# Kernel tuning notes

Measured on AMD Instinct MI355X. Metric: run time of the kernel, lower is better.

The kernel has to match this reference:

```python
import jax, jax.numpy as jnp
import numpy as np

TOP_K = 2  # config.moe_config.top_k


def setup_inputs() -> dict:
    key = jax.random.key(0)
    k0, k1, k2, k3 = jax.random.split(key, 4)
    T, H, I, E = 8192, 2048, 1408, 8  # tokens, hidden, moe_intermediate, experts
    x = jax.random.normal(k0, (T, H), jnp.float32)
    router_weight = jax.random.normal(k1, (E, H), jnp.float32) * 0.02
    gate_up_proj = jax.random.normal(k2, (E, H, 2 * I), jnp.float32) * 0.02
    down_proj = jax.random.normal(k3, (E, I, H), jnp.float32) * 0.02
    return {"x": x, "router_weight": router_weight,
            "gate_up_proj": gate_up_proj, "down_proj": down_proj}


def _moe_forward(x, router_weight, gate_up_proj, down_proj):
    # Router: fp32 gating linear (no bias), softmax over experts, top-k,
    # then scatter the top-k softmax weights into a dense [T, E] gate tensor
    # (topk_version=False path of Router.top_k_softmax).
    T = x.shape[0]
    E = router_weight.shape[0]
    logits = x.astype(jnp.float32) @ router_weight.T            # [T, E]
    probs = jax.nn.softmax(logits, axis=-1)                      # [T, E]
    topk_w, topk_idx = jax.lax.top_k(probs, TOP_K)               # [T, k]
    gates = jnp.zeros_like(logits).at[
        jnp.arange(T)[:, None], topk_idx].set(topk_w)            # [T, E] sparse gates

    # Grouped expert MLP (GroupedMLP): merged gate/up GEMM, SwiGLU, down GEMM.
    # Dispatch/permute + grouped GEMM + weighted combine is mathematically
    # out[t] = sum_e gates[t, e] * MLP_e(x[t]); expressed here as a fixed loop
    # over the small expert set with masked accumulation (jit-friendly).
    out = jnp.zeros_like(x)
    for e in range(E):
        gu = x @ gate_up_proj[e]                                 # [T, 2I]
        g, u = jnp.split(gu, 2, axis=-1)
        h = (jax.nn.silu(g) * u) @ down_proj[e]                  # [T, H]
        out = out + gates[:, e:e + 1].astype(x.dtype) * h
    return out


def reference(x, router_weight, gate_up_proj, down_proj):
    return _moe_forward(x, router_weight, gate_up_proj, down_proj)
```

## Files before the change

kernel.cpp:

```cpp
#include <hip/hip_runtime.h>
#include <hip/hip_bf16.h>
#include <cstdint>
#include <cstddef>

#define T_TOK 8192
#define H_DIM 2048
#define I_DIM 1408
#define E_NUM 8
#define BM 128
#define BK 64
#define ROWS_CAP (2 * T_TOK + E_NUM * BM)
#define MAX_MT (ROWS_CAP / BM)
#define NT1 (I_DIM / 64)
#define NT2 (H_DIM / 128)

typedef __attribute__((ext_vector_type(8))) short short8;
typedef __attribute__((ext_vector_type(4))) float f32x4;
typedef __attribute__((ext_vector_type(8))) unsigned short bf16x8;
typedef __attribute__((ext_vector_type(4))) unsigned short bf16x4;
typedef __attribute__((ext_vector_type(8))) _Float16 h16x8;

static __device__ __forceinline__ unsigned short f2bf(float f) {
  unsigned u = __float_as_uint(f);
  u += 0x7FFFu + ((u >> 16) & 1u);
  return (unsigned short)(u >> 16);
}

static __device__ __forceinline__ void gld_lds16(const void* g, void* l) {
  __builtin_amdgcn_global_load_lds(
      (__attribute__((address_space(1))) unsigned int*)g,
      (__attribute__((address_space(3))) unsigned int*)l, 16, 0, 0);
}

template <int G>
static __device__ __forceinline__ void remap_tile(int bid, int nb, int nt_cols,
                                                  int& m_t, int& n_t) {
  int chunk = nb >> 3;
  int wg = (bid & 7) * chunk + (bid >> 3);
  int grp = wg / (nt_cols * G);
  int rem = wg % (nt_cols * G);
  n_t = rem / G;
  m_t = grp * G + rem % G;
}

__global__ __launch_bounds__(256) void router_kernel(
    const float* __restrict__ x, const float* __restrict__ rw,
    unsigned short* __restrict__ xb,
    int* __restrict__ topk_idx, float* __restrict__ topk_w, int* __restrict__ meta) {
  int t = blockIdx.x * 4 + (threadIdx.x >> 6);
  int lane = threadIdx.x & 63;
  const float* xr = x + (size_t)t * H_DIM;
  unsigned short* xbr = xb + (size_t)t * H_DIM;
  float acc[E_NUM];
#pragma unroll
  for (int e = 0; e < E_NUM; e++) acc[e] = 0.f;
  for (int j = lane * 4; j < H_DIM; j += 256) {
    f32x4 v = *(const f32x4*)(xr + j);
    bf16x4 b;
#pragma unroll
    for (int u = 0; u < 4; u++) b[u] = f2bf(v[u]);
    *(bf16x4*)(xbr + j) = b;
#pragma unroll
    for (int e = 0; e < E_NUM; e++) {
      f32x4 w = *(const f32x4*)(rw + e * H_DIM + j);
      acc[e] += v[0] * w[0] + v[1] * w[1] + v[2] * w[2] + v[3] * w[3];
    }
  }
#pragma unroll
  for (int e = 0; e < E_NUM; e++) {
    float v = acc[e];
#pragma unroll
    for (int s = 32; s > 0; s >>= 1) v += __shfl_xor(v, s);
    acc[e] = v;
  }
  if (lane == 0) {
    int i0 = 0;
#pragma unroll
    for (int e = 1; e < E_NUM; e++) if (acc[e] > acc[i0]) i0 = e;
    int i1 = (i0 == 0) ? 1 : 0;
#pragma unroll
    for (int e = 0; e < E_NUM; e++) if (e != i0 && acc[e] > acc[i1]) i1 = e;
    float mx = acc[0];
#pragma unroll
    for (int e = 1; e < E_NUM; e++) mx = fmaxf(mx, acc[e]);
    float sum = 0.f, p[E_NUM];
#pragma unroll
    for (int e = 0; e < E_NUM; e++) { p[e] = expf(acc[e] - mx); sum += p[e]; }
    float inv = 1.f / sum;
    topk_idx[t * 2] = i0;  topk_idx[t * 2 + 1] = i1;
    topk_w[t * 2] = p[i0] * inv;  topk_w[t * 2 + 1] = p[i1] * inv;
    atomicAdd(&meta[i0], 1);
    atomicAdd(&meta[i1], 1);
  }
}

__global__ void scan_kernel(int* __restrict__ meta, int* __restrict__ row_token) {
  __shared__ int s_off[E_NUM + 1];
  if (threadIdx.x == 0) {
    int o = 0, nt = 0;
    for (int e = 0; e < E_NUM; e++) {
      meta[16 + e] = o; s_off[e] = o;
      int c = meta[e];
      int mtc = (c + BM - 1) / BM;
      for (int m = 0; m < mtc; m++) { meta[64 + nt] = e; meta[256 + nt] = o + m * BM; nt++; }
      o += mtc * BM;
      meta[8 + e] = 0;
    }
    meta[16 + E_NUM] = o; s_off[E_NUM] = o;
    meta[32] = nt;
  }
  __syncthreads();
  for (int e = 0; e < E_NUM; e++) {
    int lo = s_off[e] + meta[e], hi = s_off[e + 1];
    for (int r = lo + (int)threadIdx.x; r < hi; r += 64) row_token[r] = -1;
  }
}

__global__ __launch_bounds__(256) void bucket_kernel(
    const int* __restrict__ topk_idx, int* __restrict__ meta,
    int* __restrict__ row_token, int* __restrict__ tok2row) {
  int i = blockIdx.x * 256 + threadIdx.x;
  if (i >= 2 * T_TOK) return;
  int e = topk_idx[i];
  int pos = atomicAdd(&meta[8 + e], 1);
  int r = meta[16 + e] + pos;
  row_token[r] = i >> 1;
  tok2row[i] = r;
}

__global__ __launch_bounds__(256) void tcvt2_kernel(
    const float* __restrict__ wgu, const float* __restrict__ wdn,
    unsigned short* __restrict__ wgu_t, unsigned short* __restrict__ wd_t) {
  __shared__ alignas(16) float st[128 * 128];
  int z = blockIdx.z;
  const float* src; unsigned short* dst; int R, C;
  if (z < E_NUM) {
    R = H_DIM; C = 2 * I_DIM;
    src = wgu + (size_t)z * R * C;  dst = wgu_t + (size_t)z * R * C;
  } else {
    R = I_DIM; C = H_DIM;
    src = wdn + (size_t)(z - E_NUM) * R * C;  dst = wd_t + (size_t)(z - E_NUM) * R * C;
  }
  int c0 = blockIdx.x * 128, r0 = blockIdx.y * 128;
  if (c0 >= C || r0 >= R) return;
  int tid = threadIdx.x, l = tid & 63, w = tid >> 6;
#pragma unroll
  for (int i = 0; i < 16; i++) {
    int r = i * 8 + w * 2 + (l >> 5);
    int key = (r & 7) ^ ((r >> 3) & 7);
    int c4 = (l & 31) ^ key;
    gld_lds16(src + (size_t)(r0 + r) * C + c0 + c4 * 4,
              (char*)st + (i * 8 + w * 2) * 512);
  }
  __syncthreads();
  int ca = tid & 15, cg = tid >> 4;
#pragma unroll
  for (int it = 0; it < 8; it++) {
    int c = it * 16 + cg;
    bf16x8 o;
#pragma unroll
    for (int j = 0; j < 8; j++) {
      int r = ca * 8 + j;
      int key = (r & 7) ^ ((r >> 3) & 7);
      o[j] = f2bf(st[r * 128 + (((c >> 2) ^ key) << 2) + (c & 3)]);
    }
    *(bf16x8*)(dst + (size_t)(c0 + c) * R + r0 + ca * 8) = o;
  }
}

__global__ __launch_bounds__(256) void gemm1_kernel(
    const unsigned short* __restrict__ xb,
    const unsigned short* __restrict__ wgu,
    unsigned short* __restrict__ hbuf,
    const int* __restrict__ row_token, const int* __restrict__ meta) {
  int m_t, n_t;
  remap_tile<4>(blockIdx.x, NT1 * MAX_MT, NT1, m_t, n_t);
  if (m_t >= meta[32]) return;
  int e = meta[64 + m_t];
  int row0 = meta[256 + m_t];
  int n0h = n_t * 64;

  __shared__ alignas(16) char smem[65536];

  int tid = threadIdx.x, lane = tid & 63, wid = tid >> 6;
  const unsigned short* asrc[4];
  const unsigned short* bsrc[4];
  {
    const unsigned short* wb = wgu + (size_t)e * (2 * (size_t)I_DIM) * H_DIM;
#pragma unroll
    for (int i = 0; i < 4; i++) {
      int r = i * 32 + (tid >> 3);
      int ch = ((tid & 7) ^ (r & 7)) * 8;
      int tok = row_token[row0 + r];
      if (tok < 0) tok = 0;
      asrc[i] = xb + (size_t)tok * H_DIM + ch;
      int wr = (r < 64) ? (n0h + r) : (I_DIM + n0h + (r - 64));
      bsrc[i] = wb + (size_t)wr * H_DIM + ch;
    }
  }
  f32x4 acc[4][4] = {};
  int mrow = (wid >> 1) * 64 + (lane & 15);
  int brow = (wid & 1) * 64 + (lane & 15);

#define STAGE1(buf, kof_)                                                     \
  {                                                                           \
    int kof = (kof_);                                                         \
    char* b = smem + (buf) * 32768;                                           \
    _Pragma("unroll") for (int i = 0; i < 4; i++) {                           \
      gld_lds16(asrc[i] + kof, b + i * 4096 + wid * 1024);                    \
      gld_lds16(bsrc[i] + kof, b + 16384 + i * 4096 + wid * 1024);            \
    }                                                                         \
  }

  constexpr int NK1 = H_DIM / BK;
  STAGE1(0, 0);
  STAGE1(1, BK);
  for (int kt = 0; kt < NK1; kt++) {
    int cur = kt & 1;
    if (kt + 1 < NK1) { asm volatile("s_waitcnt vmcnt(8)" ::: "memory"); }
    else              { asm volatile("s_waitcnt vmcnt(0)" ::: "memory"); }
    __builtin_amdgcn_s_barrier();
    const unsigned short* sA = (const unsigned short*)(smem + cur * 32768);
    const unsigned short* sB = sA + 8192;
#pragma unroll
    for (int kk = 0; kk < 2; kk++) {
      int krd = ((kk * 4 + (lane >> 4)) ^ (lane & 7)) * 8;
      short8 af[4], bf[4];
#pragma unroll
      for (int f = 0; f < 4; f++) {
        af[f] = *(const short8*)(sA + (mrow + f * 16) * BK + krd);
        bf[f] = *(const short8*)(sB + (brow + f * 16) * BK + krd);
      }
#pragma unroll
      for (int fm = 0; fm < 4; fm++)
#pragma unroll
        for (int fn = 0; fn < 4; fn++)
          acc[fm][fn] = __builtin_amdgcn_mfma_f32_16x16x32_bf16(af[fm], bf[fn], acc[fm][fn], 0, 0, 0);
    }
    asm volatile("" ::: "memory");
    __builtin_amdgcn_s_barrier();
    asm volatile("" ::: "memory");
    if (kt + 2 < NK1) STAGE1(cur, (kt + 2) * BK);
  }

  float* xw = (float*)smem + (wid >> 1) * 4096;
  if (wid & 1) {
#pragma unroll
    for (int fm = 0; fm < 4; fm++)
#pragma unroll
      for (int r = 0; r < 4; r++) {
        int mloc = fm * 16 + (lane >> 4) * 4 + r;
#pragma unroll
        for (int fn = 0; fn < 4; fn++)
          xw[mloc * 64 + fn * 16 + (lane & 15)] = acc[fm][fn][r];
      }
  }
  __syncthreads();
  if (!(wid & 1)) {
    int mbase = row0 + (wid >> 1) * 64;
#pragma unroll
    for (int fm = 0; fm < 4; fm++)
#pragma unroll
      for (int r = 0; r < 4; r++) {
        int mloc = fm * 16 + (lane >> 4) * 4 + r;
        size_t rbase = (size_t)(mbase + mloc) * I_DIM + n0h;
#pragma unroll
        for (int fn = 0; fn < 4; fn++) {
          float g = acc[fm][fn][r];
          float u = xw[mloc * 64 + fn * 16 + (lane & 15)];
          float hv = (g / (1.f + __expf(-g))) * u;
          hbuf[rbase + fn * 16 + (lane & 15)] = f2bf(hv);
        }
      }
  }
}

__global__ __launch_bounds__(256) void gemm2_kernel(
    const unsigned short* __restrict__ hbuf,
    const unsigned short* __restrict__ wd,
    _Float16* __restrict__ part,
    const int* __restrict__ meta) {
  int m_t, n_t;
  remap_tile<8>(blockIdx.x, NT2 * MAX_MT, NT2, m_t, n_t);
  if (m_t >= meta[32]) return;
  int e = meta[64 + m_t];
  int row0 = meta[256 + m_t];
  int n0 = n_t * 128;

  __shared__ alignas(16) char smem[65536];

  int tid = threadIdx.x, lane = tid & 63, wid = tid >> 6;
  const unsigned short* asrc[4];
  const unsigned short* bsrc[4];
  {
    const unsigned short* wb = wd + (size_t)e * (size_t)H_DIM * I_DIM;
#pragma unroll
    for (int i = 0; i < 4; i++) {
      int r = i * 32 + (tid >> 3);
      int ch = ((tid & 7) ^ (r & 7)) * 8;
      asrc[i] = hbuf + (size_t)(row0 + r) * I_DIM + ch;
      bsrc[i] = wb + (size_t)(n0 + r) * I_DIM + ch;
    }
  }
  f32x4 acc[4][4] = {};
  int mrow = (wid >> 1) * 64 + (lane & 15);
  int brow = (wid & 1) * 64 + (lane & 15);

  constexpr int NK2 = I_DIM / BK;
  STAGE1(0, 0);
  STAGE1(1, BK);
  for (int kt = 0; kt < NK2; kt++) {
    int cur = kt & 1;
    if (kt + 1 < NK2) { asm volatile("s_waitcnt vmcnt(8)" ::: "memory"); }
    else              { asm volatile("s_waitcnt vmcnt(0)" ::: "memory"); }
    __builtin_amdgcn_s_barrier();
    const unsigned short* sA = (const unsigned short*)(smem + cur * 32768);
    const unsigned short* sB = sA + 8192;
#pragma unroll
    for (int kk = 0; kk < 2; kk++) {
      int krd = ((kk * 4 + (lane >> 4)) ^ (lane & 7)) * 8;
      short8 af[4], bf[4];
#pragma unroll
      for (int f = 0; f < 4; f++) {
        af[f] = *(const short8*)(sA + (mrow + f * 16) * BK + krd);
        bf[f] = *(const short8*)(sB + (brow + f * 16) * BK + krd);
      }
#pragma unroll
      for (int fm = 0; fm < 4; fm++)
#pragma unroll
        for (int fn = 0; fn < 4; fn++)
          acc[fm][fn] = __builtin_amdgcn_mfma_f32_16x16x32_bf16(af[fm], bf[fn], acc[fm][fn], 0, 0, 0);
    }
    asm volatile("" ::: "memory");
    __builtin_amdgcn_s_barrier();
    asm volatile("" ::: "memory");
    if (kt + 2 < NK2) STAGE1(cur, (kt + 2) * BK);
  }
  _Float16* stg = (_Float16*)(smem + wid * 8192);
  int l15 = lane & 15;
#pragma unroll
  for (int fm = 0; fm < 4; fm++)
#pragma unroll
    for (int r = 0; r < 4; r++) {
      int mloc = fm * 16 + (lane >> 4) * 4 + r;
#pragma unroll
      for (int fn = 0; fn < 4; fn++) {
        int nl = fn * 16 + l15;
        stg[mloc * 64 + (((nl >> 3) ^ (mloc & 7)) << 3) + (nl & 7)] =
            (_Float16)acc[fm][fn][r];
      }
    }
  int m0 = (wid >> 1) * 64;
  int nbase = n0 + (wid & 1) * 64;
  int ca = lane & 7;
#pragma unroll
  for (int it = 0; it < 8; it++) {
    int mr = it * 8 + (lane >> 3);
    h16x8 v = *(const h16x8*)(stg + mr * 64 + ((ca ^ (mr & 7)) << 3));
    *(h16x8*)(part + (size_t)(row0 + m0 + mr) * H_DIM + nbase + ca * 8) = v;
  }
}

__global__ __launch_bounds__(256) void combine_kernel(
    const _Float16* __restrict__ part, const int* __restrict__ tok2row,
    const float* __restrict__ topk_w, float* __restrict__ out) {
  int t = blockIdx.x;
  int c = threadIdx.x * 8;
  int r0 = tok2row[2 * t], r1 = tok2row[2 * t + 1];
  float w0 = topk_w[2 * t], w1 = topk_w[2 * t + 1];
  h16x8 p0 = *(const h16x8*)(part + (size_t)r0 * H_DIM + c);
  h16x8 p1 = *(const h16x8*)(part + (size_t)r1 * H_DIM + c);
  float* o = out + (size_t)t * H_DIM + c;
  f32x4 lo, hi;
#pragma unroll
  for (int j = 0; j < 4; j++) lo[j] = w0 * (float)p0[j] + w1 * (float)p1[j];
#pragma unroll
  for (int j = 0; j < 4; j++) hi[j] = w0 * (float)p0[4 + j] + w1 * (float)p1[4 + j];
  *(f32x4*)o = lo;
  *(f32x4*)(o + 4) = hi;
}

extern "C" void kernel_launch(void* const* d_in, const int* in_sizes, int n_in,
                              void* d_out, int out_size, void* d_ws, size_t ws_size,
                              hipStream_t stream) {
  const float* x   = (const float*)d_in[0];
  const float* rw  = (const float*)d_in[1];
  const float* wgu = (const float*)d_in[2];
  const float* wdn = (const float*)d_in[3];
  float* out = (float*)d_out;

  char* ws = (char*)d_ws;
  size_t off = 0;
  auto alloc = [&](size_t bytes) {
    void* p = ws + off;
    off += (bytes + 255) & ~(size_t)255;
    return p;
  };
  int* meta            = (int*)alloc(4096);
  int* topk_idx        = (int*)alloc((size_t)2 * T_TOK * 4);
  float* topk_w        = (float*)alloc((size_t)2 * T_TOK * 4);
  int* tok2row         = (int*)alloc((size_t)2 * T_TOK * 4);
  int* row_token       = (int*)alloc((size_t)ROWS_CAP * 4);
  unsigned short* xb    = (unsigned short*)alloc((size_t)T_TOK * H_DIM * 2);
  unsigned short* wgu_t = (unsigned short*)alloc((size_t)E_NUM * 2 * I_DIM * H_DIM * 2);
  unsigned short* wd_t  = (unsigned short*)alloc((size_t)E_NUM * H_DIM * I_DIM * 2);
  unsigned short* hbuf  = (unsigned short*)alloc((size_t)ROWS_CAP * I_DIM * 2);
  _Float16* part = (_Float16*)wgu_t;

  if (off > ws_size) {
    (void)hipMemsetAsync(d_out, 0, (size_t)out_size * sizeof(float), stream);
    return;
  }

  (void)hipMemsetAsync(meta, 0, 4096, stream);

  tcvt2_kernel<<<dim3(22, 16, 2 * E_NUM), 256, 0, stream>>>(wgu, wdn, wgu_t, wd_t);
  router_kernel<<<T_TOK / 4, 256, 0, stream>>>(x, rw, xb, topk_idx, topk_w, meta);
  scan_kernel<<<1, 64, 0, stream>>>(meta, row_token);
  bucket_kernel<<<(2 * T_TOK + 255) / 256, 256, 0, stream>>>(topk_idx, meta, row_token, tok2row);

  gemm1_kernel<<<NT1 * MAX_MT, 256, 0, stream>>>(xb, wgu_t, hbuf, row_token, meta);
  gemm2_kernel<<<NT2 * MAX_MT, 256, 0, stream>>>(hbuf, wd_t, part, meta);
  combine_kernel<<<T_TOK, 256, 0, stream>>>(part, tok2row, topk_w, out);
}
```

Before: 718.1 us.

## Make weight transpose-convert kernel persistent with double-buffered LDS tiles

Turns the fp32-to-bf16 weight transpose kernel into a persistent grid of 2048 blocks that walk a flattened list of 128x64 tiles. Each block double-buffers tiles in LDS, issuing async global-to-LDS loads for the next tile while converting and writing the current one. The goal is to hide load latency in this memory-bound preprocessing step and to stop launching blocks that exit early at padded tile positions. In exchange it uses smaller tiles, which gives shorter contiguous output writes, and it relies on hand-placed vmcnt waits and barriers.

```diff
diff --git a/kernel.cpp b/kernel.cpp
--- a/kernel.cpp
+++ b/kernel.cpp
@@ -13,6 +13,10 @@
 #define MAX_MT (ROWS_CAP / BM)
 #define NT1 (I_DIM / 64)
 #define NT2 (H_DIM / 128)
+#define NTILE_GU (44 * 16 * E_NUM)
+#define NTILE_DN (32 * 11 * E_NUM)
+#define NTILE_TOT (NTILE_GU + NTILE_DN)
+#define TCVT_NB 2048
 
 typedef __attribute__((ext_vector_type(8))) short short8;
 typedef __attribute__((ext_vector_type(4))) float f32x4;
@@ -131,40 +135,78 @@
 __global__ __launch_bounds__(256) void tcvt2_kernel(
     const float* __restrict__ wgu, const float* __restrict__ wdn,
     unsigned short* __restrict__ wgu_t, unsigned short* __restrict__ wd_t) {
-  __shared__ alignas(16) float st[128 * 128];
-  int z = blockIdx.z;
-  const float* src; unsigned short* dst; int R, C;
-  if (z < E_NUM) {
-    R = H_DIM; C = 2 * I_DIM;
-    src = wgu + (size_t)z * R * C;  dst = wgu_t + (size_t)z * R * C;
-  } else {
-    R = I_DIM; C = H_DIM;
-    src = wdn + (size_t)(z - E_NUM) * R * C;  dst = wd_t + (size_t)(z - E_NUM) * R * C;
-  }
-  int c0 = blockIdx.x * 128, r0 = blockIdx.y * 128;
-  if (c0 >= C || r0 >= R) return;
+  __shared__ alignas(16) float st[2][128 * 64];
   int tid = threadIdx.x, l = tid & 63, w = tid >> 6;
-#pragma unroll
-  for (int i = 0; i < 16; i++) {
-    int r = i * 8 + w * 2 + (l >> 5);
-    int key = (r & 7) ^ ((r >> 3) & 7);
-    int c4 = (l & 31) ^ key;
-    gld_lds16(src + (size_t)(r0 + r) * C + c0 + c4 * 4,
-              (char*)st + (i * 8 + w * 2) * 512);
-  }
-  __syncthreads();
-  int ca = tid & 15, cg = tid >> 4;
-#pragma unroll
-  for (int it = 0; it < 8; it++) {
-    int c = it * 16 + cg;
-    bf16x8 o;
-#pragma unroll
-    for (int j = 0; j < 8; j++) {
-      int r = ca * 8 + j;
+
+  auto decode = [&](int t, const float*& src, unsigned short*& dst,
+                    int& R, int& C, int& c0, int& r0) {
+    if (t < NTILE_GU) {
+      int e = t / 704, rem = t % 704;
+      R = H_DIM; C = 2 * I_DIM;
+      c0 = (rem % 44) * 64; r0 = (rem / 44) * 128;
+      src = wgu + (size_t)e * R * C;
+      dst = wgu_t + (size_t)e * R * C;
+    } else {
+      int tt = t - NTILE_GU;
+      int e = tt / 352, rem = tt % 352;
+      R = I_DIM; C = H_DIM;
+      c0 = (rem % 32) * 64; r0 = (rem / 32) * 128;
+      src = wdn + (size_t)e * R * C;
+      dst = wd_t + (size_t)e * R * C;
+    }
+  };
+
+  auto stage = [&](int buf, int t) {
+    const float* src; unsigned short* dst; int R, C, c0, r0;
+    decode(t, src, dst, R, C, c0, r0);
+#pragma unroll
+    for (int i = 0; i < 8; i++) {
+      int rbase = w * 32 + i * 4;
+      int r = rbase + (l >> 4);
       int key = (r & 7) ^ ((r >> 3) & 7);
-      o[j] = f2bf(st[r * 128 + (((c >> 2) ^ key) << 2) + (c & 3)]);
-    }
-    *(bf16x8*)(dst + (size_t)(c0 + c) * R + r0 + ca * 8) = o;
+      int c4 = ((l & 15) ^ key) * 4;
+      gld_lds16(src + (size_t)(r0 + r) * C + c0 + c4,
+                (char*)&st[buf][0] + rbase * 256);
+    }
+  };
+
+  auto process = [&](int buf, int t) {
+    const float* src; unsigned short* dst; int R, C, c0, r0;
+    decode(t, src, dst, R, C, c0, r0);
+    int ca = tid & 15, cg = tid >> 4;
+#pragma unroll
+    for (int it = 0; it < 4; it++) {
+      int c = it * 16 + cg;
+      bf16x8 o;
+#pragma unroll
+      for (int j = 0; j < 8; j++) {
+        int r = ca * 8 + j;
+        int key = (r & 7) ^ ((r >> 3) & 7);
+        o[j] = f2bf(st[buf][r * 64 + (((c >> 2) ^ key) << 2) + (c & 3)]);
+      }
+      *(bf16x8*)(dst + (size_t)(c0 + c) * R + r0 + ca * 8) = o;
+    }
+  };
+
+  int t = blockIdx.x;
+  if (t >= NTILE_TOT) return;
+  int nxt = t + TCVT_NB;
+  stage(0, t);
+  int buf = 0;
+  while (true) {
+    bool has_next = (nxt < NTILE_TOT);
+    if (has_next) {
+      stage(buf ^ 1, nxt);
+      asm volatile("s_waitcnt vmcnt(8)" ::: "memory");
+    } else {
+      asm volatile("s_waitcnt vmcnt(0)" ::: "memory");
+    }
+    __builtin_amdgcn_s_barrier();
+    process(buf, t);
+    if (!has_next) break;
+    asm volatile("" ::: "memory");
+    __builtin_amdgcn_s_barrier();
+    t = nxt; nxt += TCVT_NB; buf ^= 1;
   }
 }
 
@@ -414,7 +456,7 @@
 
   (void)hipMemsetAsync(meta, 0, 4096, stream);
 
-  tcvt2_kernel<<<dim3(22, 16, 2 * E_NUM), 256, 0, stream>>>(wgu, wdn, wgu_t, wd_t);
+  tcvt2_kernel<<<TCVT_NB, 256, 0, stream>>>(wgu, wdn, wgu_t, wd_t);
   router_kernel<<<T_TOK / 4, 256, 0, stream>>>(x, rw, xb, topk_idx, topk_w, meta);
   scan_kernel<<<1, 64, 0, stream>>>(meta, row_token);
   bucket_kernel<<<(2 * T_TOK + 255) / 256, 256, 0, stream>>>(topk_idx, meta, row_token, tok2row);
```

Measured after the change: 726.8 us. About the same (+1.2%).
